# Optimization experiments

Measured on AMD Instinct MI355X. Metric: run time of the kernel, lower is better.

## Reference

```python
import jax, jax.numpy as jnp
import numpy as np

N = 100000
E = 6400000
DIMS = [34, 16, 16, 16, 4]


def setup_inputs() -> dict:
    key = jax.random.key(0)
    ks = jax.random.split(key, 12)
    x = jax.random.normal(ks[0], (N, DIMS[0]), dtype=jnp.float32)
    edge_index = jax.random.randint(ks[1], (2, E), 0, N, dtype=jnp.int64)
    inp = {"x": x, "edge_index": edge_index}
    for i in range(4):
        fan_in, fan_out = DIMS[i], DIMS[i + 1]
        s = (6.0 / (fan_in + fan_out)) ** 0.5  # glorot
        inp[f"W{i+1}"] = jax.random.uniform(ks[2 + 2 * i], (fan_in, fan_out), minval=-s, maxval=s, dtype=jnp.float32)
        inp[f"b{i+1}"] = jnp.zeros((fan_out,), dtype=jnp.float32)
    return inp


def gcn_layer(x, W, b, src, dst, norm):
    # x: [N, din] -> [N, dout]; PyG GCNConv: h = XW, aggregate norm*h[src] into dst, + bias
    h = x @ W
    msgs = h[src] * norm[:, None]                      # [E+N, dout]
    out = jax.ops.segment_sum(msgs, dst, num_segments=N)
    return out + b


def reference(x, edge_index, W1, b1, W2, b2, W3, b3, W4, b4):
    loop = jnp.arange(N, dtype=edge_index.dtype)
    src = jnp.concatenate([edge_index[0], loop])       # add self-loops
    dst = jnp.concatenate([edge_index[1], loop])
    deg = jax.ops.segment_sum(jnp.ones_like(dst, dtype=x.dtype), dst, num_segments=N)
    dinv = jnp.where(deg > 0, jax.lax.rsqrt(deg), 0.0)
    norm = dinv[src] * dinv[dst]                       # symmetric normalization per edge
    h = gcn_layer(x, W1, b1, src, dst, norm)
    h = jax.nn.relu(h)
    h = gcn_layer(h, W2, b2, src, dst, norm)
    h = jax.nn.relu(h)
    h = gcn_layer(h, W3, b3, src, dst, norm)
    h = jax.nn.relu(h)
    return gcn_layer(h, W4, b4, src, dst, norm)
```

## Files before the change

### kernel.cpp

```cpp
#include <hip/hip_runtime.h>
#include <hip/hip_bf16.h>


static constexpr int THREADS = 256;
static constexpr int BSHIFT  = 8;
static constexpr int NPB     = 256;
static constexpr int MAXB    = 512;
static constexpr int NCHUNK  = 512;
static constexpr int EPT     = 8;


__global__ __launch_bounds__(THREADS)
void k_hist(const int* __restrict__ dst, int* __restrict__ hist_part,
            int e, int nbkt, int chunk) {
    __shared__ int h[MAXB];
    for (int t = threadIdx.x; t < nbkt; t += THREADS) h[t] = 0;
    __syncthreads();
    int beg = blockIdx.x * chunk;
    int end = min(e, beg + chunk);
    for (int base = beg; base < end; base += THREADS * EPT) {
        int i = base + (int)threadIdx.x * EPT;
        if (i + EPT <= end) {
            int4 d0 = *(const int4*)(dst + i);
            int4 d1 = *(const int4*)(dst + i + 4);
            atomicAdd(&h[d0.x >> BSHIFT], 1);
            atomicAdd(&h[d0.y >> BSHIFT], 1);
            atomicAdd(&h[d0.z >> BSHIFT], 1);
            atomicAdd(&h[d0.w >> BSHIFT], 1);
            atomicAdd(&h[d1.x >> BSHIFT], 1);
            atomicAdd(&h[d1.y >> BSHIFT], 1);
            atomicAdd(&h[d1.z >> BSHIFT], 1);
            atomicAdd(&h[d1.w >> BSHIFT], 1);
        } else {
            for (int k = i; k < end; k++) atomicAdd(&h[dst[k] >> BSHIFT], 1);
        }
    }
    __syncthreads();
    for (int t = threadIdx.x; t < nbkt; t += THREADS)
        hist_part[(size_t)blockIdx.x * nbkt + t] = h[t];
}

__global__ __launch_bounds__(NCHUNK)
void k_colscan(int* __restrict__ hist_part, int* __restrict__ btot, int nbkt) {
    __shared__ int s[NCHUNK];
    int b = blockIdx.x;
    int v = hist_part[(size_t)threadIdx.x * nbkt + b];
    s[threadIdx.x] = v;
    __syncthreads();
    for (int ofs = 1; ofs < NCHUNK; ofs <<= 1) {
        int t = (threadIdx.x >= ofs) ? s[threadIdx.x - ofs] : 0;
        __syncthreads();
        s[threadIdx.x] += t;
        __syncthreads();
    }
    hist_part[(size_t)threadIdx.x * nbkt + b] = s[threadIdx.x] - v;
    if (threadIdx.x == NCHUNK - 1) btot[b] = s[NCHUNK - 1];
}

__global__ __launch_bounds__(1024)
void k_scan_b(const int* __restrict__ btot, int* __restrict__ bbase,
              int nbkt, int e) {
    __shared__ int s[1024];
    int v = (threadIdx.x < nbkt) ? btot[threadIdx.x] : 0;
    s[threadIdx.x] = v;
    __syncthreads();
    for (int ofs = 1; ofs < 1024; ofs <<= 1) {
        int t = (threadIdx.x >= ofs) ? s[threadIdx.x - ofs] : 0;
        __syncthreads();
        s[threadIdx.x] += t;
        __syncthreads();
    }
    if (threadIdx.x < nbkt) bbase[threadIdx.x] = s[threadIdx.x] - v;
    if (threadIdx.x == 0) bbase[nbkt] = e;
}

__global__ __launch_bounds__(THREADS)
void k_scatter_bkt(const int* __restrict__ src, const int* __restrict__ dst,
                   const int* __restrict__ offs_part, const int* __restrict__ bbase,
                   int* __restrict__ gpack, int e, int nbkt, int chunk) {
    __shared__ int curs[MAXB];
    for (int t = threadIdx.x; t < nbkt; t += THREADS)
        curs[t] = bbase[t] + offs_part[(size_t)blockIdx.x * nbkt + t];
    __syncthreads();
    int beg = blockIdx.x * chunk;
    int end = min(e, beg + chunk);
    for (int base = beg; base < end; base += THREADS * EPT) {
        int i = base + (int)threadIdx.x * EPT;
        if (i + EPT <= end) {
            int4 s0 = *(const int4*)(src + i);
            int4 s1 = *(const int4*)(src + i + 4);
            int4 d0 = *(const int4*)(dst + i);
            int4 d1 = *(const int4*)(dst + i + 4);
            int p0 = atomicAdd(&curs[d0.x >> BSHIFT], 1);
            int p1 = atomicAdd(&curs[d0.y >> BSHIFT], 1);
            int p2 = atomicAdd(&curs[d0.z >> BSHIFT], 1);
            int p3 = atomicAdd(&curs[d0.w >> BSHIFT], 1);
            int p4 = atomicAdd(&curs[d1.x >> BSHIFT], 1);
            int p5 = atomicAdd(&curs[d1.y >> BSHIFT], 1);
            int p6 = atomicAdd(&curs[d1.z >> BSHIFT], 1);
            int p7 = atomicAdd(&curs[d1.w >> BSHIFT], 1);
            gpack[p0] = (s0.x << BSHIFT) | (d0.x & (NPB - 1));
            gpack[p1] = (s0.y << BSHIFT) | (d0.y & (NPB - 1));
            gpack[p2] = (s0.z << BSHIFT) | (d0.z & (NPB - 1));
            gpack[p3] = (s0.w << BSHIFT) | (d0.w & (NPB - 1));
            gpack[p4] = (s1.x << BSHIFT) | (d1.x & (NPB - 1));
            gpack[p5] = (s1.y << BSHIFT) | (d1.y & (NPB - 1));
            gpack[p6] = (s1.z << BSHIFT) | (d1.z & (NPB - 1));
            gpack[p7] = (s1.w << BSHIFT) | (d1.w & (NPB - 1));
        } else {
            for (int k = i; k < end; k++) {
                int d = dst[k];
                int p = atomicAdd(&curs[d >> BSHIFT], 1);
                gpack[p] = (src[k] << BSHIFT) | (d & (NPB - 1));
            }
        }
    }
}

__global__ __launch_bounds__(THREADS)
void k_bucket_build(const int* __restrict__ gpack, const int* __restrict__ bbase,
                    int* __restrict__ rowptr, float* __restrict__ dinv,
                    int* __restrict__ csr, int n, int nbkt) {
    __shared__ int hist[NPB];
    __shared__ int scn[NPB];
    int b = blockIdx.x;
    int node0 = b << BSHIFT;
    int nnodes = min(NPB, n - node0);
    int ebeg = bbase[b];
    int eend = bbase[b + 1];
    int tid = threadIdx.x;

    hist[tid] = 0;
    __syncthreads();
    for (int i = ebeg + tid; i < eend; i += THREADS)
        atomicAdd(&hist[gpack[i] & (NPB - 1)], 1);
    __syncthreads();
    scn[tid] = hist[tid];
    __syncthreads();
    for (int ofs = 1; ofs < NPB; ofs <<= 1) {
        int t = (tid >= ofs) ? scn[tid - ofs] : 0;
        __syncthreads();
        scn[tid] += t;
        __syncthreads();
    }
    if (tid < nnodes) {
        int h = hist[tid];
        int excl = scn[tid] - h;
        rowptr[node0 + tid] = ebeg + excl;
        dinv[node0 + tid] = 1.0f / sqrtf((float)(h + 1));
    }
    if (b == nbkt - 1 && tid == 0) rowptr[n] = eend;
    scn[tid] = ebeg + (scn[tid] - hist[tid]);
    __syncthreads();
    for (int i = ebeg + tid; i < eend; i += THREADS) {
        int g = gpack[i];
        int pos = atomicAdd(&scn[g & (NPB - 1)], 1);
        csr[pos] = g >> BSHIFT;
    }
}


template<int DIN, int DOUT, bool TRANSFORM>
__global__ __launch_bounds__(THREADS)
void k_layer(const float* __restrict__ in, const float* __restrict__ W,
             const float* __restrict__ bprev, const float* __restrict__ dinv,
             float* __restrict__ hp, int n) {
    __shared__ float sW[DIN * DOUT];
    for (int t = threadIdx.x; t < DIN * DOUT; t += THREADS) sW[t] = W[t];
    __syncthreads();

    int i = blockIdx.x * THREADS + threadIdx.x;
    if (i >= n) return;
    float di = dinv[i];

    float xin[DIN];
    if constexpr (DIN % 4 == 0) {
        const float4* in4 = (const float4*)(in + (size_t)i * DIN);
        #pragma unroll
        for (int k4 = 0; k4 < DIN / 4; k4++) {
            float4 v = in4[k4];
            xin[4 * k4 + 0] = v.x; xin[4 * k4 + 1] = v.y;
            xin[4 * k4 + 2] = v.z; xin[4 * k4 + 3] = v.w;
        }
    } else {
        #pragma unroll
        for (int k = 0; k < DIN; k++) xin[k] = in[(size_t)i * DIN + k];
    }
    if constexpr (TRANSFORM) {
        #pragma unroll
        for (int k = 0; k < DIN; k++)
            xin[k] = fmaxf(fmaf(di, xin[k], bprev[k]), 0.0f);
    }

    float acc[DOUT];
    #pragma unroll
    for (int j = 0; j < DOUT; j++) acc[j] = 0.0f;
    #pragma unroll
    for (int k = 0; k < DIN; k++) {
        float xk = xin[k];
        #pragma unroll
        for (int j = 0; j < DOUT; j++) acc[j] = fmaf(xk, sW[k * DOUT + j], acc[j]);
    }

    float4* hp4 = (float4*)(hp + (size_t)i * DOUT);
    #pragma unroll
    for (int j4 = 0; j4 < DOUT / 4; j4++)
        hp4[j4] = make_float4(acc[4 * j4] * di, acc[4 * j4 + 1] * di,
                              acc[4 * j4 + 2] * di, acc[4 * j4 + 3] * di);
}

template<int D, bool FINAL>
__global__ __launch_bounds__(THREADS)
void k_gather(const int* __restrict__ rowptr, const int* __restrict__ csr,
              const float* __restrict__ hp, float* __restrict__ outp,
              const float* __restrict__ dinv, const float* __restrict__ bias,
              int n) {
    int tid  = blockIdx.x * THREADS + threadIdx.x;
    int row  = tid / D;
    int lane = tid & (D - 1);
    if (row >= n) return;
    int base = (threadIdx.x & 63) & ~(D - 1);

    int beg = rowptr[row];
    int end = rowptr[row + 1];

    float a0 = hp[(size_t)row * D + lane];
    float a1 = 0.f, a2 = 0.f, a3 = 0.f;

    int e = beg;
    for (; e + D <= end; e += D) {
        int s = csr[e + lane];
        #pragma unroll
        for (int k = 0; k < D; k += 4) {
            int s0 = __shfl(s, base + k + 0, 64);
            int s1 = __shfl(s, base + k + 1, 64);
            int s2 = __shfl(s, base + k + 2, 64);
            int s3 = __shfl(s, base + k + 3, 64);
            a0 += hp[(size_t)s0 * D + lane];
            a1 += hp[(size_t)s1 * D + lane];
            a2 += hp[(size_t)s2 * D + lane];
            a3 += hp[(size_t)s3 * D + lane];
        }
    }
    if (e < end) {
        int idx = e + lane;
        int s = (idx < end) ? csr[idx] : 0;
        int cnt = end - e;
        for (int k = 0; k < cnt; k++) {
            int sk = __shfl(s, base + k, 64);
            a0 += hp[(size_t)sk * D + lane];
        }
    }
    float acc = (a0 + a1) + (a2 + a3);

    if constexpr (FINAL) {
        outp[(size_t)row * D + lane] = fmaf(dinv[row], acc, bias[lane]);
    } else {
        outp[(size_t)row * D + lane] = acc;
    }
}


__global__ __launch_bounds__(THREADS)
void k_zero(int* __restrict__ p, int n) {
    int i = blockIdx.x * THREADS + threadIdx.x;
    if (i < n) p[i] = 0;
}

__global__ __launch_bounds__(THREADS)
void k_count_deg(const int* __restrict__ dst, int* __restrict__ deg, int e) {
    int i = blockIdx.x * THREADS + threadIdx.x;
    if (i >= e) return;
    atomicAdd(&deg[dst[i]], 1);
}

__global__ __launch_bounds__(THREADS)
void k_dinv(const int* __restrict__ deg, float* __restrict__ dinv, int n) {
    int i = blockIdx.x * THREADS + threadIdx.x;
    if (i < n) dinv[i] = 1.0f / sqrtf((float)(deg[i] + 1));
}

__global__ __launch_bounds__(THREADS)
void k_scan1(const int* __restrict__ deg, int* __restrict__ rowptr,
             int* __restrict__ bsum, int n) {
    __shared__ int s[THREADS];
    int i = blockIdx.x * THREADS + threadIdx.x;
    int v = (i < n) ? deg[i] : 0;
    s[threadIdx.x] = v;
    __syncthreads();
    for (int ofs = 1; ofs < THREADS; ofs <<= 1) {
        int t = (threadIdx.x >= ofs) ? s[threadIdx.x - ofs] : 0;
        __syncthreads();
        s[threadIdx.x] += t;
        __syncthreads();
    }
    if (i < n) rowptr[i] = s[threadIdx.x] - v;
    if (threadIdx.x == THREADS - 1) bsum[blockIdx.x] = s[THREADS - 1];
}

__global__ __launch_bounds__(1024)
void k_scan2(int* __restrict__ bsum, int nb) {
    __shared__ int s[1024];
    int v = (threadIdx.x < nb) ? bsum[threadIdx.x] : 0;
    s[threadIdx.x] = v;
    __syncthreads();
    for (int ofs = 1; ofs < 1024; ofs <<= 1) {
        int t = (threadIdx.x >= ofs) ? s[threadIdx.x - ofs] : 0;
        __syncthreads();
        s[threadIdx.x] += t;
        __syncthreads();
    }
    if (threadIdx.x < nb) bsum[threadIdx.x] = s[threadIdx.x] - v;
}

__global__ __launch_bounds__(THREADS)
void k_scan3(int* __restrict__ rowptr, const int* __restrict__ bsum,
             int* __restrict__ cursor, int n, int e) {
    int i = blockIdx.x * THREADS + threadIdx.x;
    if (i < n) {
        int r = rowptr[i] + bsum[blockIdx.x];
        rowptr[i] = r;
        cursor[i] = r;
    }
    if (i == 0) rowptr[n] = e;
}

__global__ __launch_bounds__(THREADS)
void k_fill_cursor(const int* __restrict__ src, const int* __restrict__ dst,
                   int* __restrict__ cursor, int* __restrict__ csr, int e) {
    int i = blockIdx.x * THREADS + threadIdx.x;
    if (i >= e) return;
    int pos = atomicAdd(&cursor[dst[i]], 1);
    csr[pos] = src[i];
}


extern "C" void kernel_launch(void* const* d_in, const int* in_sizes, int n_in,
                              void* d_out, int out_size, void* d_ws, size_t ws_size,
                              hipStream_t stream) {
    const float* x   = (const float*)d_in[0];
    const int*   ei  = (const int*)d_in[1];
    const float* W1  = (const float*)d_in[2];
    const float* b1  = (const float*)d_in[3];
    const float* W2  = (const float*)d_in[4];
    const float* b2  = (const float*)d_in[5];
    const float* W3  = (const float*)d_in[6];
    const float* b3  = (const float*)d_in[7];
    const float* W4  = (const float*)d_in[8];
    const float* b4  = (const float*)d_in[9];
    float*       out = (float*)d_out;

    const int N = in_sizes[0] / 34;
    const int E = in_sizes[1] / 2;
    const int* src = ei;
    const int* dst = ei + E;

    const int gN  = (N + THREADS - 1) / THREADS;
    const int g16 = (int)(((size_t)N * 16 + THREADS - 1) / THREADS);
    const int g4  = (int)(((size_t)N * 4 + THREADS - 1) / THREADS);

    const int nbkt  = (N + NPB - 1) >> BSHIFT;
    const int chunk = (((E + NCHUNK - 1) / NCHUNK) + EPT - 1) & ~(EPT - 1);

    {
        char* ws = (char*)d_ws;
        size_t off = 0;
        auto alloc = [&](size_t bytes) -> void* {
            void* p = ws + off;
            off += (bytes + 255) & ~(size_t)255;
            return p;
        };
        float* dinv   = (float*)alloc((size_t)N * 4);
        float* bufA   = (float*)alloc((size_t)N * 16 * 4);
        float* bufB   = (float*)alloc((size_t)N * 16 * 4);
        int*   rowptr = (int*)  alloc((size_t)(N + 1) * 4);
        int*   csr    = (int*)  alloc((size_t)E * 4);
        int*   gpack  = (int*)  alloc((size_t)E * 4);
        int*   offsp  = (int*)  alloc((size_t)NCHUNK * nbkt * 4);
        int*   btot   = (int*)  alloc((size_t)nbkt * 4);
        int*   bbase  = (int*)  alloc((size_t)(nbkt + 1) * 4);

        bool aligned16 = (((uintptr_t)src & 15) == 0) && (((uintptr_t)dst & 15) == 0);
        bool fast_ok = (nbkt <= MAXB) && (off <= ws_size) && aligned16 &&
                       (N <= (1 << (31 - BSHIFT)));

        if (fast_ok) {
            k_hist       <<<NCHUNK, THREADS, 0, stream>>>(dst, offsp, E, nbkt, chunk);
            k_colscan    <<<nbkt, NCHUNK, 0, stream>>>(offsp, btot, nbkt);
            k_scan_b     <<<1, 1024, 0, stream>>>(btot, bbase, nbkt, E);
            k_scatter_bkt<<<NCHUNK, THREADS, 0, stream>>>(src, dst, offsp, bbase,
                                                          gpack, E, nbkt, chunk);
            k_bucket_build<<<nbkt, THREADS, 0, stream>>>(gpack, bbase, rowptr,
                                                         dinv, csr, N, nbkt);

            k_layer<34, 16, false><<<gN, THREADS, 0, stream>>>(x, W1, nullptr, dinv, bufA, N);
            k_gather<16, false><<<g16, THREADS, 0, stream>>>(rowptr, csr, bufA, bufB, nullptr, nullptr, N);

            k_layer<16, 16, true><<<gN, THREADS, 0, stream>>>(bufB, W2, b1, dinv, bufA, N);
            k_gather<16, false><<<g16, THREADS, 0, stream>>>(rowptr, csr, bufA, bufB, nullptr, nullptr, N);

            k_layer<16, 16, true><<<gN, THREADS, 0, stream>>>(bufB, W3, b2, dinv, bufA, N);
            k_gather<16, false><<<g16, THREADS, 0, stream>>>(rowptr, csr, bufA, bufB, nullptr, nullptr, N);

            k_layer<16, 4, true><<<gN, THREADS, 0, stream>>>(bufB, W4, b3, dinv, bufA, N);
            k_gather<4, true><<<g4, THREADS, 0, stream>>>(rowptr, csr, bufA, out, dinv, b4, N);
            return;
        }
    }

    {
        char* ws = (char*)d_ws;
        size_t off = 0;
        auto alloc = [&](size_t bytes) -> void* {
            void* p = ws + off;
            off += (bytes + 255) & ~(size_t)255;
            return p;
        };
        int*   deg    = (int*)  alloc((size_t)N * 4);
        float* dinv   = (float*)alloc((size_t)N * 4);
        float* bufA   = (float*)alloc((size_t)N * 16 * 4);
        float* bufB   = (float*)alloc((size_t)N * 16 * 4);
        int*   rowptr = (int*)  alloc((size_t)(N + 1) * 4);
        int*   cursor = (int*)  alloc((size_t)N * 4);
        const int nb  = (N + THREADS - 1) / THREADS;
        int*   bsum   = (int*)  alloc((size_t)nb * 4);
        int*   csr    = (int*)  alloc((size_t)E * 4);

        const int gE = (E + THREADS - 1) / THREADS;

        k_zero<<<gN, THREADS, 0, stream>>>(deg, N);
        k_count_deg<<<gE, THREADS, 0, stream>>>(dst, deg, E);
        k_dinv<<<gN, THREADS, 0, stream>>>(deg, dinv, N);
        k_scan1<<<nb, THREADS, 0, stream>>>(deg, rowptr, bsum, N);
        k_scan2<<<1, 1024, 0, stream>>>(bsum, nb);
        k_scan3<<<nb, THREADS, 0, stream>>>(rowptr, bsum, cursor, N, E);
        k_fill_cursor<<<gE, THREADS, 0, stream>>>(src, dst, cursor, csr, E);

        k_layer<34, 16, false><<<gN, THREADS, 0, stream>>>(x, W1, nullptr, dinv, bufA, N);
        k_gather<16, false><<<g16, THREADS, 0, stream>>>(rowptr, csr, bufA, bufB, nullptr, nullptr, N);

        k_layer<16, 16, true><<<gN, THREADS, 0, stream>>>(bufB, W2, b1, dinv, bufA, N);
        k_gather<16, false><<<g16, THREADS, 0, stream>>>(rowptr, csr, bufA, bufB, nullptr, nullptr, N);

        k_layer<16, 16, true><<<gN, THREADS, 0, stream>>>(bufB, W3, b2, dinv, bufA, N);
        k_gather<16, false><<<g16, THREADS, 0, stream>>>(rowptr, csr, bufA, bufB, nullptr, nullptr, N);

        k_layer<16, 4, true><<<gN, THREADS, 0, stream>>>(bufB, W4, b3, dinv, bufA, N);
        k_gather<4, true><<<g4, THREADS, 0, stream>>>(rowptr, csr, bufA, out, dinv, b4, N);
    }
}
```

Before: 382.9 us.

## Split 16-wide node features into two 8-wide planes gathered separately

Hidden features are stored as two separate N×8 planes instead of one N×16 buffer. Each aggregation layer now runs two 8-lane gather passes, one per plane, so each pass touches a smaller random-access working set that may fit in L2. The dense-transform kernels are specialised to read and write the planar layout. The cost is that CSR indices and row pointers are read twice per layer, there are extra kernel launches, and each gathered row segment is only 32 bytes.

```diff
diff --git a/kernel.cpp b/kernel.cpp
--- a/kernel.cpp
+++ b/kernel.cpp
@@ -160,6 +160,279 @@
 }
 
 
+__global__ __launch_bounds__(THREADS)
+void k_layer_in(const float* __restrict__ x, const float* __restrict__ W,
+                const float* __restrict__ dinv,
+                float* __restrict__ hp0, float* __restrict__ hp1, int n) {
+    __shared__ float sW[34 * 16];
+    for (int t = threadIdx.x; t < 34 * 16; t += THREADS) sW[t] = W[t];
+    __syncthreads();
+    int i = blockIdx.x * THREADS + threadIdx.x;
+    if (i >= n) return;
+    float di = dinv[i];
+    float acc[16];
+    #pragma unroll
+    for (int j = 0; j < 16; j++) acc[j] = 0.0f;
+    const float* xi = x + (size_t)i * 34;
+    #pragma unroll
+    for (int k = 0; k < 34; k++) {
+        float xk = xi[k];
+        #pragma unroll
+        for (int j = 0; j < 16; j++) acc[j] = fmaf(xk, sW[k * 16 + j], acc[j]);
+    }
+    float4* p0 = (float4*)(hp0 + (size_t)i * 8);
+    float4* p1 = (float4*)(hp1 + (size_t)i * 8);
+    p0[0] = make_float4(acc[0] * di, acc[1] * di, acc[2] * di, acc[3] * di);
+    p0[1] = make_float4(acc[4] * di, acc[5] * di, acc[6] * di, acc[7] * di);
+    p1[0] = make_float4(acc[8] * di, acc[9] * di, acc[10] * di, acc[11] * di);
+    p1[1] = make_float4(acc[12] * di, acc[13] * di, acc[14] * di, acc[15] * di);
+}
+
+__global__ __launch_bounds__(THREADS)
+void k_layer_mid(const float* __restrict__ ag0, const float* __restrict__ ag1,
+                 const float* __restrict__ W, const float* __restrict__ bprev,
+                 const float* __restrict__ dinv,
+                 float* __restrict__ hp0, float* __restrict__ hp1, int n) {
+    __shared__ float sW[16 * 16];
+    __shared__ float sB[16];
+    for (int t = threadIdx.x; t < 16 * 16; t += THREADS) sW[t] = W[t];
+    if (threadIdx.x < 16) sB[threadIdx.x] = bprev[threadIdx.x];
+    __syncthreads();
+    int i = blockIdx.x * THREADS + threadIdx.x;
+    if (i >= n) return;
+    float di = dinv[i];
+    float xin[16];
+    {
+        const float4* a0 = (const float4*)(ag0 + (size_t)i * 8);
+        const float4* a1 = (const float4*)(ag1 + (size_t)i * 8);
+        float4 v;
+        v = a0[0]; xin[0] = v.x; xin[1] = v.y; xin[2] = v.z; xin[3] = v.w;
+        v = a0[1]; xin[4] = v.x; xin[5] = v.y; xin[6] = v.z; xin[7] = v.w;
+        v = a1[0]; xin[8] = v.x; xin[9] = v.y; xin[10] = v.z; xin[11] = v.w;
+        v = a1[1]; xin[12] = v.x; xin[13] = v.y; xin[14] = v.z; xin[15] = v.w;
+    }
+    #pragma unroll
+    for (int k = 0; k < 16; k++)
+        xin[k] = fmaxf(fmaf(di, xin[k], sB[k]), 0.0f);
+    float acc[16];
+    #pragma unroll
+    for (int j = 0; j < 16; j++) acc[j] = 0.0f;
+    #pragma unroll
+    for (int k = 0; k < 16; k++) {
+        float xk = xin[k];
+        #pragma unroll
+        for (int j = 0; j < 16; j++) acc[j] = fmaf(xk, sW[k * 16 + j], acc[j]);
+    }
+    float4* p0 = (float4*)(hp0 + (size_t)i * 8);
+    float4* p1 = (float4*)(hp1 + (size_t)i * 8);
+    p0[0] = make_float4(acc[0] * di, acc[1] * di, acc[2] * di, acc[3] * di);
+    p0[1] = make_float4(acc[4] * di, acc[5] * di, acc[6] * di, acc[7] * di);
+    p1[0] = make_float4(acc[8] * di, acc[9] * di, acc[10] * di, acc[11] * di);
+    p1[1] = make_float4(acc[12] * di, acc[13] * di, acc[14] * di, acc[15] * di);
+}
+
+__global__ __launch_bounds__(THREADS)
+void k_layer_last(const float* __restrict__ ag0, const float* __restrict__ ag1,
+                  const float* __restrict__ W, const float* __restrict__ bprev,
+                  const float* __restrict__ dinv, float* __restrict__ hp4, int n) {
+    __shared__ float sW[16 * 4];
+    __shared__ float sB[16];
+    for (int t = threadIdx.x; t < 16 * 4; t += THREADS) sW[t] = W[t];
+    if (threadIdx.x < 16) sB[threadIdx.x] = bprev[threadIdx.x];
+    __syncthreads();
+    int i = blockIdx.x * THREADS + threadIdx.x;
+    if (i >= n) return;
+    float di = dinv[i];
+    float xin[16];
+    {
+        const float4* a0 = (const float4*)(ag0 + (size_t)i * 8);
+        const float4* a1 = (const float4*)(ag1 + (size_t)i * 8);
+        float4 v;
+        v = a0[0]; xin[0] = v.x; xin[1] = v.y; xin[2] = v.z; xin[3] = v.w;
+        v = a0[1]; xin[4] = v.x; xin[5] = v.y; xin[6] = v.z; xin[7] = v.w;
+        v = a1[0]; xin[8] = v.x; xin[9] = v.y; xin[10] = v.z; xin[11] = v.w;
+        v = a1[1]; xin[12] = v.x; xin[13] = v.y; xin[14] = v.z; xin[15] = v.w;
+    }
+    #pragma unroll
+    for (int k = 0; k < 16; k++)
+        xin[k] = fmaxf(fmaf(di, xin[k], sB[k]), 0.0f);
+    float acc[4];
+    #pragma unroll
+    for (int j = 0; j < 4; j++) acc[j] = 0.0f;
+    #pragma unroll
+    for (int k = 0; k < 16; k++) {
+        float xk = xin[k];
+        #pragma unroll
+        for (int j = 0; j < 4; j++) acc[j] = fmaf(xk, sW[k * 4 + j], acc[j]);
+    }
+    *(float4*)(hp4 + (size_t)i * 4) =
+        make_float4(acc[0] * di, acc[1] * di, acc[2] * di, acc[3] * di);
+}
+
+
+__global__ __launch_bounds__(THREADS)
+void k_gather8(const int* __restrict__ rowptr, const int* __restrict__ csr,
+               const float* __restrict__ plane, float* __restrict__ outp, int n) {
+    int tid  = blockIdx.x * THREADS + threadIdx.x;
+    int row  = tid >> 3;
+    int lane = tid & 7;
+    if (row >= n) return;
+    int base = (threadIdx.x & 63) & ~7;
+
+    int beg = rowptr[row];
+    int end = rowptr[row + 1];
+
+    float a0 = plane[(size_t)row * 8 + lane];
+    float a1 = 0.f, a2 = 0.f, a3 = 0.f;
+
+    int e = beg;
+    for (; e + 8 <= end; e += 8) {
+        int s = csr[e + lane];
+        int s0 = __shfl(s, base + 0, 64);
+        int s1 = __shfl(s, base + 1, 64);
+        int s2 = __shfl(s, base + 2, 64);
+        int s3 = __shfl(s, base + 3, 64);
+        int s4 = __shfl(s, base + 4, 64);
+        int s5 = __shfl(s, base + 5, 64);
+        int s6 = __shfl(s, base + 6, 64);
+        int s7 = __shfl(s, base + 7, 64);
+        a0 += plane[(size_t)s0 * 8 + lane];
+        a1 += plane[(size_t)s1 * 8 + lane];
+        a2 += plane[(size_t)s2 * 8 + lane];
+        a3 += plane[(size_t)s3 * 8 + lane];
+        a0 += plane[(size_t)s4 * 8 + lane];
+        a1 += plane[(size_t)s5 * 8 + lane];
+        a2 += plane[(size_t)s6 * 8 + lane];
+        a3 += plane[(size_t)s7 * 8 + lane];
+    }
+    if (e < end) {
+        int idx = e + lane;
+        int s = (idx < end) ? csr[idx] : 0;
+        int cnt = end - e;
+        for (int k = 0; k < cnt; k++) {
+            int sk = __shfl(s, base + k, 64);
+            a0 += plane[(size_t)sk * 8 + lane];
+        }
+    }
+    outp[(size_t)row * 8 + lane] = (a0 + a1) + (a2 + a3);
+}
+
+__global__ __launch_bounds__(THREADS)
+void k_gather4_final(const int* __restrict__ rowptr, const int* __restrict__ csr,
+                     const float* __restrict__ hp, float* __restrict__ outp,
+                     const float* __restrict__ dinv, const float* __restrict__ bias,
+                     int n) {
+    int tid  = blockIdx.x * THREADS + threadIdx.x;
+    int row  = tid >> 2;
+    int lane = tid & 3;
+    if (row >= n) return;
+    int base = (threadIdx.x & 63) & ~3;
+
+    int beg = rowptr[row];
+    int end = rowptr[row + 1];
+
+    float a0 = hp[(size_t)row * 4 + lane];
+    float a1 = 0.f, a2 = 0.f, a3 = 0.f;
+
+    int e = beg;
+    for (; e + 4 <= end; e += 4) {
+        int s = csr[e + lane];
+        int s0 = __shfl(s, base + 0, 64);
+        int s1 = __shfl(s, base + 1, 64);
+        int s2 = __shfl(s, base + 2, 64);
+        int s3 = __shfl(s, base + 3, 64);
+        a0 += hp[(size_t)s0 * 4 + lane];
+        a1 += hp[(size_t)s1 * 4 + lane];
+        a2 += hp[(size_t)s2 * 4 + lane];
+        a3 += hp[(size_t)s3 * 4 + lane];
+    }
+    if (e < end) {
+        int idx = e + lane;
+        int s = (idx < end) ? csr[idx] : 0;
+        int cnt = end - e;
+        for (int k = 0; k < cnt; k++) {
+            int sk = __shfl(s, base + k, 64);
+            a0 += hp[(size_t)sk * 4 + lane];
+        }
+    }
+    float acc = (a0 + a1) + (a2 + a3);
+    outp[(size_t)row * 4 + lane] = fmaf(dinv[row], acc, bias[lane]);
+}
+
+
+__global__ __launch_bounds__(THREADS)
+void k_zero(int* __restrict__ p, int n) {
+    int i = blockIdx.x * THREADS + threadIdx.x;
+    if (i < n) p[i] = 0;
+}
+
+__global__ __launch_bounds__(THREADS)
+void k_count_deg(const int* __restrict__ dst, int* __restrict__ deg, int e) {
+    int i = blockIdx.x * THREADS + threadIdx.x;
+    if (i >= e) return;
+    atomicAdd(&deg[dst[i]], 1);
+}
+
+__global__ __launch_bounds__(THREADS)
+void k_dinv(const int* __restrict__ deg, float* __restrict__ dinv, int n) {
+    int i = blockIdx.x * THREADS + threadIdx.x;
+    if (i < n) dinv[i] = 1.0f / sqrtf((float)(deg[i] + 1));
+}
+
+__global__ __launch_bounds__(THREADS)
+void k_scan1(const int* __restrict__ deg, int* __restrict__ rowptr,
+             int* __restrict__ bsum, int n) {
+    __shared__ int s[THREADS];
+    int i = blockIdx.x * THREADS + threadIdx.x;
+    int v = (i < n) ? deg[i] : 0;
+    s[threadIdx.x] = v;
+    __syncthreads();
+    for (int ofs = 1; ofs < THREADS; ofs <<= 1) {
+        int t = (threadIdx.x >= ofs) ? s[threadIdx.x - ofs] : 0;
+        __syncthreads();
+        s[threadIdx.x] += t;
+        __syncthreads();
+    }
+    if (i < n) rowptr[i] = s[threadIdx.x] - v;
+    if (threadIdx.x == THREADS - 1) bsum[blockIdx.x] = s[THREADS - 1];
+}
+
+__global__ __launch_bounds__(1024)
+void k_scan2(int* __restrict__ bsum, int nb) {
+    __shared__ int s[1024];
+    int v = (threadIdx.x < nb) ? bsum[threadIdx.x] : 0;
+    s[threadIdx.x] = v;
+    __syncthreads();
+    for (int ofs = 1; ofs < 1024; ofs <<= 1) {
+        int t = (threadIdx.x >= ofs) ? s[threadIdx.x - ofs] : 0;
+        __syncthreads();
+        s[threadIdx.x] += t;
+        __syncthreads();
+    }
+    if (threadIdx.x < nb) bsum[threadIdx.x] = s[threadIdx.x] - v;
+}
+
+__global__ __launch_bounds__(THREADS)
+void k_scan3(int* __restrict__ rowptr, const int* __restrict__ bsum,
+             int* __restrict__ cursor, int n, int e) {
+    int i = blockIdx.x * THREADS + threadIdx.x;
+    if (i < n) {
+        int r = rowptr[i] + bsum[blockIdx.x];
+        rowptr[i] = r;
+        cursor[i] = r;
+    }
+    if (i == 0) rowptr[n] = e;
+}
+
+__global__ __launch_bounds__(THREADS)
+void k_fill_cursor(const int* __restrict__ src, const int* __restrict__ dst,
+                   int* __restrict__ cursor, int* __restrict__ csr, int e) {
+    int i = blockIdx.x * THREADS + threadIdx.x;
+    if (i >= e) return;
+    int pos = atomicAdd(&cursor[dst[i]], 1);
+    csr[pos] = src[i];
+}
+
 template<int DIN, int DOUT, bool TRANSFORM>
 __global__ __launch_bounds__(THREADS)
 void k_layer(const float* __restrict__ in, const float* __restrict__ W,
@@ -168,30 +441,17 @@
     __shared__ float sW[DIN * DOUT];
     for (int t = threadIdx.x; t < DIN * DOUT; t += THREADS) sW[t] = W[t];
     __syncthreads();
-
     int i = blockIdx.x * THREADS + threadIdx.x;
     if (i >= n) return;
     float di = dinv[i];
-
     float xin[DIN];
-    if constexpr (DIN % 4 == 0) {
-        const float4* in4 = (const float4*)(in + (size_t)i * DIN);
-        #pragma unroll
-        for (int k4 = 0; k4 < DIN / 4; k4++) {
-            float4 v = in4[k4];
-            xin[4 * k4 + 0] = v.x; xin[4 * k4 + 1] = v.y;
-            xin[4 * k4 + 2] = v.z; xin[4 * k4 + 3] = v.w;
-        }
-    } else {
-        #pragma unroll
-        for (int k = 0; k < DIN; k++) xin[k] = in[(size_t)i * DIN + k];
-    }
+    #pragma unroll
+    for (int k = 0; k < DIN; k++) xin[k] = in[(size_t)i * DIN + k];
     if constexpr (TRANSFORM) {
         #pragma unroll
         for (int k = 0; k < DIN; k++)
             xin[k] = fmaxf(fmaf(di, xin[k], bprev[k]), 0.0f);
     }
-
     float acc[DOUT];
     #pragma unroll
     for (int j = 0; j < DOUT; j++) acc[j] = 0.0f;
@@ -201,12 +461,8 @@
         #pragma unroll
         for (int j = 0; j < DOUT; j++) acc[j] = fmaf(xk, sW[k * DOUT + j], acc[j]);
     }
-
-    float4* hp4 = (float4*)(hp + (size_t)i * DOUT);
-    #pragma unroll
-    for (int j4 = 0; j4 < DOUT / 4; j4++)
-        hp4[j4] = make_float4(acc[4 * j4] * di, acc[4 * j4 + 1] * di,
-                              acc[4 * j4 + 2] * di, acc[4 * j4 + 3] * di);
+    #pragma unroll
+    for (int j = 0; j < DOUT; j++) hp[(size_t)i * DOUT + j] = acc[j] * di;
 }
 
 template<int D, bool FINAL>
@@ -220,13 +476,10 @@
     int lane = tid & (D - 1);
     if (row >= n) return;
     int base = (threadIdx.x & 63) & ~(D - 1);
-
     int beg = rowptr[row];
     int end = rowptr[row + 1];
-
     float a0 = hp[(size_t)row * D + lane];
     float a1 = 0.f, a2 = 0.f, a3 = 0.f;
-
     int e = beg;
     for (; e + D <= end; e += D) {
         int s = csr[e + lane];
@@ -252,86 +505,11 @@
         }
     }
     float acc = (a0 + a1) + (a2 + a3);
-
     if constexpr (FINAL) {
         outp[(size_t)row * D + lane] = fmaf(dinv[row], acc, bias[lane]);
     } else {
         outp[(size_t)row * D + lane] = acc;
     }
-}
-
-
-__global__ __launch_bounds__(THREADS)
-void k_zero(int* __restrict__ p, int n) {
-    int i = blockIdx.x * THREADS + threadIdx.x;
-    if (i < n) p[i] = 0;
-}
-
-__global__ __launch_bounds__(THREADS)
-void k_count_deg(const int* __restrict__ dst, int* __restrict__ deg, int e) {
-    int i = blockIdx.x * THREADS + threadIdx.x;
-    if (i >= e) return;
-    atomicAdd(&deg[dst[i]], 1);
-}
-
-__global__ __launch_bounds__(THREADS)
-void k_dinv(const int* __restrict__ deg, float* __restrict__ dinv, int n) {
-    int i = blockIdx.x * THREADS + threadIdx.x;
-    if (i < n) dinv[i] = 1.0f / sqrtf((float)(deg[i] + 1));
-}
-
-__global__ __launch_bounds__(THREADS)
-void k_scan1(const int* __restrict__ deg, int* __restrict__ rowptr,
-             int* __restrict__ bsum, int n) {
-    __shared__ int s[THREADS];
-    int i = blockIdx.x * THREADS + threadIdx.x;
-    int v = (i < n) ? deg[i] : 0;
-    s[threadIdx.x] = v;
-    __syncthreads();
-    for (int ofs = 1; ofs < THREADS; ofs <<= 1) {
-        int t = (threadIdx.x >= ofs) ? s[threadIdx.x - ofs] : 0;
-        __syncthreads();
-        s[threadIdx.x] += t;
-        __syncthreads();
-    }
-    if (i < n) rowptr[i] = s[threadIdx.x] - v;
-    if (threadIdx.x == THREADS - 1) bsum[blockIdx.x] = s[THREADS - 1];
-}
-
-__global__ __launch_bounds__(1024)
-void k_scan2(int* __restrict__ bsum, int nb) {
-    __shared__ int s[1024];
-    int v = (threadIdx.x < nb) ? bsum[threadIdx.x] : 0;
-    s[threadIdx.x] = v;
-    __syncthreads();
-    for (int ofs = 1; ofs < 1024; ofs <<= 1) {
-        int t = (threadIdx.x >= ofs) ? s[threadIdx.x - ofs] : 0;
-        __syncthreads();
-        s[threadIdx.x] += t;
-        __syncthreads();
-    }
-    if (threadIdx.x < nb) bsum[threadIdx.x] = s[threadIdx.x] - v;
-}
-
-__global__ __launch_bounds__(THREADS)
-void k_scan3(int* __restrict__ rowptr, const int* __restrict__ bsum,
-             int* __restrict__ cursor, int n, int e) {
-    int i = blockIdx.x * THREADS + threadIdx.x;
-    if (i < n) {
-        int r = rowptr[i] + bsum[blockIdx.x];
-        rowptr[i] = r;
-        cursor[i] = r;
-    }
-    if (i == 0) rowptr[n] = e;
-}
-
-__global__ __launch_bounds__(THREADS)
-void k_fill_cursor(const int* __restrict__ src, const int* __restrict__ dst,
-                   int* __restrict__ cursor, int* __restrict__ csr, int e) {
-    int i = blockIdx.x * THREADS + threadIdx.x;
-    if (i >= e) return;
-    int pos = atomicAdd(&cursor[dst[i]], 1);
-    csr[pos] = src[i];
 }
 
 
@@ -356,7 +534,7 @@
     const int* dst = ei + E;
 
     const int gN  = (N + THREADS - 1) / THREADS;
-    const int g16 = (int)(((size_t)N * 16 + THREADS - 1) / THREADS);
+    const int g8  = (int)(((size_t)N * 8 + THREADS - 1) / THREADS);
     const int g4  = (int)(((size_t)N * 4 + THREADS - 1) / THREADS);
 
     const int nbkt  = (N + NPB - 1) >> BSHIFT;
@@ -371,8 +549,11 @@
             return p;
         };
         float* dinv   = (float*)alloc((size_t)N * 4);
-        float* bufA   = (float*)alloc((size_t)N * 16 * 4);
-        float* bufB   = (float*)alloc((size_t)N * 16 * 4);
+        float* hpP0   = (float*)alloc((size_t)N * 8 * 4);
+        float* hpP1   = (float*)alloc((size_t)N * 8 * 4);
+        float* agP0   = (float*)alloc((size_t)N * 8 * 4);
+        float* agP1   = (float*)alloc((size_t)N * 8 * 4);
+        float* hp4    = (float*)alloc((size_t)N * 4 * 4);
         int*   rowptr = (int*)  alloc((size_t)(N + 1) * 4);
         int*   csr    = (int*)  alloc((size_t)E * 4);
         int*   gpack  = (int*)  alloc((size_t)E * 4);
@@ -393,17 +574,20 @@
             k_bucket_build<<<nbkt, THREADS, 0, stream>>>(gpack, bbase, rowptr,
                                                          dinv, csr, N, nbkt);
 
-            k_layer<34, 16, false><<<gN, THREADS, 0, stream>>>(x, W1, nullptr, dinv, bufA, N);
-            k_gather<16, false><<<g16, THREADS, 0, stream>>>(rowptr, csr, bufA, bufB, nullptr, nullptr, N);
-
-            k_layer<16, 16, true><<<gN, THREADS, 0, stream>>>(bufB, W2, b1, dinv, bufA, N);
-            k_gather<16, false><<<g16, THREADS, 0, stream>>>(rowptr, csr, bufA, bufB, nullptr, nullptr, N);
-
-            k_layer<16, 16, true><<<gN, THREADS, 0, stream>>>(bufB, W3, b2, dinv, bufA, N);
-            k_gather<16, false><<<g16, THREADS, 0, stream>>>(rowptr, csr, bufA, bufB, nullptr, nullptr, N);
-
-            k_layer<16, 4, true><<<gN, THREADS, 0, stream>>>(bufB, W4, b3, dinv, bufA, N);
-            k_gather<4, true><<<g4, THREADS, 0, stream>>>(rowptr, csr, bufA, out, dinv, b4, N);
+            k_layer_in<<<gN, THREADS, 0, stream>>>(x, W1, dinv, hpP0, hpP1, N);
+            k_gather8<<<g8, THREADS, 0, stream>>>(rowptr, csr, hpP0, agP0, N);
+            k_gather8<<<g8, THREADS, 0, stream>>>(rowptr, csr, hpP1, agP1, N);
+
+            k_layer_mid<<<gN, THREADS, 0, stream>>>(agP0, agP1, W2, b1, dinv, hpP0, hpP1, N);
+            k_gather8<<<g8, THREADS, 0, stream>>>(rowptr, csr, hpP0, agP0, N);
+            k_gather8<<<g8, THREADS, 0, stream>>>(rowptr, csr, hpP1, agP1, N);
+
+            k_layer_mid<<<gN, THREADS, 0, stream>>>(agP0, agP1, W3, b2, dinv, hpP0, hpP1, N);
+            k_gather8<<<g8, THREADS, 0, stream>>>(rowptr, csr, hpP0, agP0, N);
+            k_gather8<<<g8, THREADS, 0, stream>>>(rowptr, csr, hpP1, agP1, N);
+
+            k_layer_last<<<gN, THREADS, 0, stream>>>(agP0, agP1, W4, b3, dinv, hp4, N);
+            k_gather4_final<<<g4, THREADS, 0, stream>>>(rowptr, csr, hp4, out, dinv, b4, N);
             return;
         }
     }
@@ -426,7 +610,8 @@
         int*   bsum   = (int*)  alloc((size_t)nb * 4);
         int*   csr    = (int*)  alloc((size_t)E * 4);
 
-        const int gE = (E + THREADS - 1) / THREADS;
+        const int gE  = (E + THREADS - 1) / THREADS;
+        const int g16 = (int)(((size_t)N * 16 + THREADS - 1) / THREADS);
 
         k_zero<<<gN, THREADS, 0, stream>>>(deg, N);
         k_count_deg<<<gE, THREADS, 0, stream>>>(dst, deg, E);
```

Result: slower. 435.7 us (+13.8%).
